# Optimization experiments

Hardware: AMD Instinct MI355X
Metric: run time of the kernel (lower is better)

The kernel has to match this reference:

```python
import jax, jax.numpy as jnp
import numpy as np

N = 512          # max_nodes
H = 256          # hidden_dim
L = 4            # num_layers
T = 100          # num_timesteps
NE = N * (N - 1) // 2  # 130816 upper-triangular edges

# --- cosine noise schedule (computed in float64 numpy, stored as float32) ---
_s = 0.008
_steps = np.arange(T + 1, dtype=np.float64)
_ab = np.cos((_steps / T + _s) / (1 + _s) * np.pi / 2) ** 2
_ab = _ab / _ab[0]
_betas = np.clip(1.0 - _ab[1:] / _ab[:-1], None, 0.999).astype(np.float32)
_alphas = 1.0 - _betas
_alpha_bar = np.cumprod(_alphas).astype(np.float32)
SQRT_AB = jnp.asarray(np.sqrt(_alpha_bar), dtype=jnp.float32)
SQRT_OMAB = jnp.asarray(np.sqrt(1.0 - _alpha_bar), dtype=jnp.float32)
IU, JU = np.triu_indices(N, k=1)  # upper-triangular edge indices


def silu(x):
    return x * jax.nn.sigmoid(x)


def layernorm(x, g, b, eps=1e-5):
    mu = jnp.mean(x, axis=-1, keepdims=True)
    var = jnp.mean(jnp.square(x - mu), axis=-1, keepdims=True)
    return (x - mu) / jnp.sqrt(var + eps) * g + b


def setup_inputs() -> dict:
    key = jax.random.key(0)
    ks = jax.random.split(key, 16)
    B = 32
    p = lambda k, shape: jax.random.normal(k, shape, dtype=jnp.float32) * 0.02
    return {
        "adj_0": jax.random.normal(ks[0], (B, N, N), dtype=jnp.float32),
        "noise": jax.random.normal(ks[1], (B, N, N), dtype=jnp.float32),
        # time embedding MLP: Linear(1,H), SiLU, Linear(H,H)
        "te_W1": p(ks[2], (1, H)), "te_b1": jnp.zeros((H,), jnp.float32),
        "te_W2": p(ks[3], (H, H)), "te_b2": jnp.zeros((H,), jnp.float32),
        # input projection Linear(N, H)
        "ip_W": p(ks[4], (N, H)), "ip_b": jnp.zeros((H,), jnp.float32),
        # per-layer params stacked on leading L axis
        "msg_W": p(ks[5], (L, H, H)), "msg_b": jnp.zeros((L, H), jnp.float32),
        "upd_W": p(ks[6], (L, 2 * H, H)), "upd_b": jnp.zeros((L, H), jnp.float32),
        "ln_g": jnp.ones((L, H), jnp.float32), "ln_b": jnp.zeros((L, H), jnp.float32),
        "tp_W": p(ks[7], (L, H, H)), "tp_b": jnp.zeros((L, H), jnp.float32),
        # output projection: Linear(H,H), SiLU, Linear(H, NE)
        "op_W1": p(ks[8], (H, H)), "op_b1": jnp.zeros((H,), jnp.float32),
        "op_W2": p(ks[9], (H, NE)), "op_b2": jnp.zeros((NE,), jnp.float32),
        "t": jax.random.randint(ks[10], (32,), 0, T),
    }


def reference(adj_0, noise, te_W1, te_b1, te_W2, te_b2, ip_W, ip_b,
              msg_W, msg_b, upd_W, upd_b, ln_g, ln_b, tp_W, tp_b,
              op_W1, op_b1, op_W2, op_b2, t):
    # q_sample: noisy adjacency at timestep t
    adj_t = SQRT_AB[t][:, None, None] * adj_0 + SQRT_OMAB[t][:, None, None] * noise
    # time embedding
    tf = (t.astype(jnp.float32) / T)[:, None]               # [B,1]
    t_emb = silu(tf @ te_W1 + te_b1) @ te_W2 + te_b2        # [B,H]
    # input projection
    h = adj_t @ ip_W + ip_b                                  # [B,N,H]
    # adjacency normalization is identical across layers -> hoist
    adj_norm = adj_t / (jnp.sum(jnp.abs(adj_t), axis=-1, keepdims=True) + 1.0)
    for l in range(L):
        msg = jnp.einsum('bij,bjh->bih', adj_norm, h @ msg_W[l] + msg_b[l])
        t_bias = (t_emb @ tp_W[l] + tp_b[l])[:, None, :]     # [B,1,H]
        h_new = jnp.concatenate([h, msg], axis=-1) @ upd_W[l] + upd_b[l] + t_bias
        h = layernorm(h_new + h, ln_g[l], ln_b[l])
    h_graph = jnp.sum(h, axis=1)                             # [B,H]
    noise_pred = silu(h_graph @ op_W1 + op_b1) @ op_W2 + op_b2  # [B,NE]
    # MSE against the upper-triangular entries of the true noise
    target = noise[:, IU, JU]                                # [B,NE]
    loss = jnp.mean(jnp.square(noise_pred - target))
    return loss
```

## Files before the change

### kernel.cpp

```cpp
#include <hip/hip_runtime.h>
#include <math.h>

#define NN 512
#define HH 256
#define BB 32
#define NE 130816

typedef unsigned short ushort_t;
typedef unsigned int u32;
using short8  = __attribute__((ext_vector_type(8))) short;
using floatx4 = __attribute__((ext_vector_type(4))) float;

typedef __attribute__((address_space(3))) u32* lds_u32p;
typedef const __attribute__((address_space(1))) u32* glb_u32p;

__device__ inline unsigned short f2bf(float f) {
    unsigned int u = __float_as_uint(f);
    unsigned int r = (u + 0x7fffu + ((u >> 16) & 1u)) >> 16;
    return (unsigned short)r;
}
__device__ inline float bf2f(unsigned short x) {
    return __uint_as_float(((unsigned int)x) << 16);
}

__device__ inline float wave_reduce_sum(float v) {
#pragma unroll
    for (int o = 32; o > 0; o >>= 1) v += __shfl_xor(v, o, 64);
    return v;
}
__device__ inline float block_reduce_sum256(float v, float* red) {
    v = wave_reduce_sum(v);
    int w = threadIdx.x >> 6;
    if ((threadIdx.x & 63) == 0) red[w] = v;
    __syncthreads();
    v = red[0] + red[1] + red[2] + red[3];
    __syncthreads();
    return v;
}

__global__ void init_kernel(float* __restrict__ sched, float* __restrict__ out) {
    __shared__ float alpha_s[100];
    int tid = threadIdx.x;
    if (tid < 100) {
        const double PI_H = 3.14159265358979323846 * 0.5;
        double f1 = (((double)tid / 100.0) + 0.008) / 1.008 * PI_H;
        double f2 = (((double)(tid + 1) / 100.0) + 0.008) / 1.008 * PI_H;
        double c1 = cos(f1), c2 = cos(f2);
        double beta = 1.0 - (c2 * c2) / (c1 * c1);
        if (beta > 0.999) beta = 0.999;
        alpha_s[tid] = 1.0f - (float)beta;
    }
    __syncthreads();
    if (tid == 0) {
        out[0] = 0.0f;
        float cum = 1.0f;
        for (int k = 0; k < 100; k++) {
            cum *= alpha_s[k];
            sched[k]       = sqrtf(cum);
            sched[100 + k] = sqrtf(1.0f - cum);
        }
    }
}

__global__ __launch_bounds__(256) void temb1_kernel(
    const float* __restrict__ te_W1, const float* __restrict__ te_b1,
    const float* __restrict__ te_W2, const float* __restrict__ te_b2,
    const int* __restrict__ t, float* __restrict__ emb_out) {
    const int b = blockIdx.x, cb = blockIdx.y * 64, tid = threadIdx.x;
    __shared__ float hid[HH];
    __shared__ float part[4][64];
    float tf = (float)t[b] / 100.0f;
    float z = tf * te_W1[tid] + te_b1[tid];
    hid[tid] = z / (1.0f + expf(-z));
    __syncthreads();
    const int col = tid & 63, kc = tid >> 6;
    float a = 0.0f;
#pragma unroll 8
    for (int k0 = 0; k0 < 64; k0++) {
        int k = kc * 64 + k0;
        a = fmaf(hid[k], te_W2[k * HH + cb + col], a);
    }
    part[kc][col] = a;
    __syncthreads();
    if (kc == 0) {
        float o = part[0][col] + part[1][col] + part[2][col] + part[3][col] + te_b2[cb + col];
        emb_out[b * HH + cb + col] = o;
    }
}

__global__ __launch_bounds__(256) void temb2_kernel(
    const float* __restrict__ emb, const float* __restrict__ tp_W,
    const float* __restrict__ tp_b, float* __restrict__ tbias_out) {
    const int b = blockIdx.x;
    const int l = blockIdx.y >> 2, cb = (blockIdx.y & 3) * 64;
    const int tid = threadIdx.x;
    __shared__ float es[HH];
    __shared__ float part[4][64];
    es[tid] = emb[b * HH + tid];
    __syncthreads();
    const int col = tid & 63, kc = tid >> 6;
    const float* W = tp_W + l * HH * HH;
    float a = 0.0f;
#pragma unroll 8
    for (int k0 = 0; k0 < 64; k0++) {
        int k = kc * 64 + k0;
        a = fmaf(es[k], W[k * HH + cb + col], a);
    }
    part[kc][col] = a;
    __syncthreads();
    if (kc == 0) {
        float o = part[0][col] + part[1][col] + part[2][col] + part[3][col]
                + tp_b[l * HH + cb + col];
        tbias_out[l * (BB * HH) + b * HH + cb + col] = o;
    }
}

__global__ __launch_bounds__(256) void adj_kernel(
    const float* __restrict__ adj0, const float* __restrict__ noise,
    const int* __restrict__ t, const float* __restrict__ sched,
    ushort_t* __restrict__ adjt_bf, float* __restrict__ invrs) {
    __shared__ float red[4];
    const int bid = blockIdx.x;
    const int b = bid >> 9;
    const int ts = t[b];
    const float sab = sched[ts], som = sched[100 + ts];
    const size_t base = (size_t)bid * NN;
    const int tid = threadIdx.x;
    float s = 0.0f;
#pragma unroll
    for (int jj = 0; jj < 2; jj++) {
        int j = tid + jj * 256;
        float a = sab * adj0[base + j] + som * noise[base + j];
        adjt_bf[base + j] = f2bf(a);
        s += fabsf(a);
    }
    s = block_reduce_sum256(s, red);
    if (tid == 0) invrs[bid] = 1.0f / (s + 1.0f);
}

__global__ __launch_bounds__(256) void wcvt_kernel(
    const float* __restrict__ ip_W, const float* __restrict__ msg_W,
    const float* __restrict__ upd_W,
    ushort_t* __restrict__ ipWT, ushort_t* __restrict__ msgWT,
    ushort_t* __restrict__ updWT) {
    const int z = blockIdx.z;
    const float* src; ushort_t* dst; int R;
    if (z == 0)      { src = ip_W;                          dst = ipWT;                       R = 512; }
    else if (z <= 4) { src = msg_W + (z - 1) * 65536;       dst = msgWT + (z - 1) * 65536;    R = 256; }
    else             { src = upd_W + (z - 5) * 131072;      dst = updWT + (z - 5) * 131072;   R = 512; }
    const int r0 = blockIdx.y * 32, c0 = blockIdx.x * 32;
    if (r0 >= R) return;
    __shared__ float T[32][33];
    const int tr = threadIdx.x >> 5, tc = threadIdx.x & 31;
#pragma unroll
    for (int s = 0; s < 32; s += 8)
        T[tr + s][tc] = src[(size_t)(r0 + tr + s) * 256 + c0 + tc];
    __syncthreads();
#pragma unroll
    for (int s = 0; s < 32; s += 8)
        dst[(size_t)(c0 + tr + s) * R + r0 + tc] = f2bf(T[tc][tr + s]);
}

__global__ __launch_bounds__(256, 2) void gemm_bf16(
    int K,
    const ushort_t* __restrict__ A, int lda, const ushort_t* __restrict__ A2,
    const ushort_t* __restrict__ BT, int ldbt, long long bstride,
    const float* __restrict__ bias, const float* __restrict__ scale,
    const float* __restrict__ tbias, const ushort_t* __restrict__ resid,
    float* __restrict__ Cf, ushort_t* __restrict__ Cb, ushort_t* __restrict__ CbT) {
    __shared__ ushort_t As[128 * 32];
    __shared__ ushort_t Bs[64 * 32];
    __shared__ ushort_t Ts[64 * 136];
    const int row0 = blockIdx.x * 128;
    const int n0 = blockIdx.y * 64;
    const int tid = threadIdx.x;
    const int lane = tid & 63;
    const int w = tid >> 6;
    const int l15 = lane & 15, quad = lane >> 4;
    const int wm = (w >> 1) * 64, wn = (w & 1) * 32;
    const ushort_t* Bp = BT + (size_t)(row0 >> 9) * (size_t)bstride;

    const int srow = lane >> 2;
    const int gkoff = (((lane & 3) ^ (lane >> 4)) << 3);
    const int swz = ((quad ^ ((l15 >> 2) & 3)) << 3);

    floatx4 acc[4][2];
#pragma unroll
    for (int i = 0; i < 4; i++)
#pragma unroll
        for (int j = 0; j < 2; j++) {
            acc[i][j][0] = 0.0f; acc[i][j][1] = 0.0f;
            acc[i][j][2] = 0.0f; acc[i][j][3] = 0.0f;
        }

    for (int kc = 0; kc < K; kc += 32) {
        const ushort_t* Ause = A; int kk = kc;
        if (A2 && kc >= 256) { Ause = A2; kk = kc - 256; }
#pragma unroll
        for (int r = 0; r < 2; r++) {
            const int lbase = (r * 4 + w) * 16;
            const ushort_t* gpA = Ause + (size_t)(row0 + lbase + srow) * lda + kk + gkoff;
            __builtin_amdgcn_global_load_lds((glb_u32p)(const void*)gpA,
                                             (lds_u32p)(void*)&As[lbase * 32], 16, 0, 0);
        }
        {
            const int lbase = w * 16;
            const ushort_t* gpB = Bp + (size_t)(n0 + lbase + srow) * ldbt + kc + gkoff;
            __builtin_amdgcn_global_load_lds((glb_u32p)(const void*)gpB,
                                             (lds_u32p)(void*)&Bs[lbase * 32], 16, 0, 0);
        }
        __syncthreads();

        short8 af[4], bfr[2];
#pragma unroll
        for (int tm = 0; tm < 4; tm++)
            af[tm] = *(const short8*)&As[(wm + tm * 16 + l15) * 32 + swz];
#pragma unroll
        for (int tn = 0; tn < 2; tn++)
            bfr[tn] = *(const short8*)&Bs[(wn + tn * 16 + l15) * 32 + swz];
#pragma unroll
        for (int tm = 0; tm < 4; tm++)
#pragma unroll
            for (int tn = 0; tn < 2; tn++)
                acc[tm][tn] = __builtin_amdgcn_mfma_f32_16x16x32_bf16(
                    af[tm], bfr[tn], acc[tm][tn], 0, 0, 0);
        __syncthreads();
    }

    if (CbT) {
#pragma unroll
        for (int tm = 0; tm < 4; tm++)
#pragma unroll
            for (int tn = 0; tn < 2; tn++)
#pragma unroll
                for (int r = 0; r < 4; r++) {
                    const int ml = wm + tm * 16 + quad * 4 + r;
                    const int cl = wn + tn * 16 + l15;
                    float v = acc[tm][tn][r];
                    if (bias) v += bias[n0 + cl];
                    Ts[cl * 136 + ml] = f2bf(v);
                }
        __syncthreads();
        const int cl = tid >> 2, ch = (tid & 3) * 32;
        const int b = row0 >> 9;
        ushort_t* dst = CbT + (size_t)b * NN * HH + (size_t)(n0 + cl) * NN + (row0 & 511) + ch;
        uint4 u0 = *(const uint4*)&Ts[cl * 136 + ch];
        uint4 u1 = *(const uint4*)&Ts[cl * 136 + ch + 8];
        uint4 u2 = *(const uint4*)&Ts[cl * 136 + ch + 16];
        uint4 u3 = *(const uint4*)&Ts[cl * 136 + ch + 24];
        *(uint4*)(dst)      = u0;
        *(uint4*)(dst + 8)  = u1;
        *(uint4*)(dst + 16) = u2;
        *(uint4*)(dst + 24) = u3;
        return;
    }

#pragma unroll
    for (int tm = 0; tm < 4; tm++)
#pragma unroll
        for (int tn = 0; tn < 2; tn++) {
#pragma unroll
            for (int r = 0; r < 4; r++) {
                const int row = row0 + wm + tm * 16 + quad * 4 + r;
                const int col = n0 + wn + tn * 16 + l15;
                float v = acc[tm][tn][r];
                if (scale) v *= scale[row];
                if (bias) v += bias[col];
                if (tbias) v += tbias[((row >> 9) << 8) + col] + bf2f(resid[(size_t)row * HH + col]);
                if (Cf) Cf[(size_t)row * HH + col] = v;
                if (Cb) Cb[(size_t)row * HH + col] = f2bf(v);
            }
        }
}

__global__ __launch_bounds__(256) void ln_kernel(
    const float* __restrict__ pre, const float* __restrict__ g,
    const float* __restrict__ b, ushort_t* __restrict__ h_bf) {
    __shared__ float red[4];
    const size_t base = (size_t)blockIdx.x * HH;
    const int tid = threadIdx.x;
    float x = pre[base + tid];
    float mu = block_reduce_sum256(x, red) * (1.0f / HH);
    float d = x - mu;
    float var = block_reduce_sum256(d * d, red) * (1.0f / HH);
    h_bf[base + tid] = f2bf(d * rsqrtf(var + 1e-5f) * g[tid] + b[tid]);
}

__global__ __launch_bounds__(256) void psum_kernel(
    const ushort_t* __restrict__ h_bf, float* __restrict__ partial) {
    const int b = blockIdx.x, ch = blockIdx.y, tid = threadIdx.x;
    const ushort_t* hp = h_bf + ((size_t)b * NN + ch * 32) * HH;
    float s = 0.0f;
#pragma unroll
    for (int i = 0; i < 32; i++) s += bf2f(hp[i * HH + tid]);
    partial[(((size_t)b * 16 + ch) << 8) + tid] = s;
}

__global__ __launch_bounds__(256) void final_kernel(
    const float* __restrict__ partial, const float* __restrict__ op_W1,
    const float* __restrict__ op_b1, float* __restrict__ sT) {
    int b = blockIdx.x, tid = threadIdx.x;
    __shared__ float hg[HH];
    float acc = 0.0f;
#pragma unroll
    for (int c = 0; c < 16; c++) acc += partial[(((size_t)b * 16 + c) << 8) + tid];
    hg[tid] = acc;
    __syncthreads();
    float o = op_b1[tid];
#pragma unroll 8
    for (int k = 0; k < HH; k++) o = fmaf(hg[k], op_W1[k * HH + tid], o);
    sT[tid * BB + b] = o / (1.0f + expf(-o));
}

__global__ __launch_bounds__(256) void loss_kernel(
    const float* __restrict__ sT, const float* __restrict__ op_W2,
    const float* __restrict__ op_b2, const float* __restrict__ noise,
    float* __restrict__ out) {
    __shared__ float red[4];
    const int tid = threadIdx.x;
    const int e = blockIdx.x * 256 + tid;
    float lsum = 0.0f;
    float acc[32];
#pragma unroll
    for (int b = 0; b < 32; b++) acc[b] = 0.0f;
    const float* w2 = op_W2 + e;
#pragma unroll 8
    for (int h = 0; h < 256; h++) {
        float wv = w2[(size_t)h * NE];
        const float* sr = sT + h * BB;
#pragma unroll
        for (int b = 0; b < 32; b++) acc[b] = fmaf(sr[b], wv, acc[b]);
    }
    int i = (int)((1023.0 - sqrt(1046529.0 - 8.0 * (double)e)) * 0.5);
    if (i < 0) i = 0;
    if (i > 510) i = 510;
    while (i > 0 && (i * (1023 - i)) / 2 > e) --i;
    while (((i + 1) * (1022 - i)) / 2 <= e) ++i;
    int j = i + 1 + (e - (i * (1023 - i)) / 2);
    const float pb = op_b2[e];
    const float* np = noise + (size_t)i * NN + j;
#pragma unroll
    for (int b = 0; b < 32; b++) {
        float d = acc[b] + pb - np[(size_t)b * NN * NN];
        lsum += d * d;
    }
    lsum *= (1.0f / (32.0f * (float)NE));
    lsum = block_reduce_sum256(lsum, red);
    if (tid == 0) atomicAdd(out, lsum);
}

extern "C" void kernel_launch(void* const* d_in, const int* in_sizes, int n_in,
                              void* d_out, int out_size, void* d_ws, size_t ws_size,
                              hipStream_t stream) {
    const float* adj0  = (const float*)d_in[0];
    const float* noise = (const float*)d_in[1];
    const float* te_W1 = (const float*)d_in[2];
    const float* te_b1 = (const float*)d_in[3];
    const float* te_W2 = (const float*)d_in[4];
    const float* te_b2 = (const float*)d_in[5];
    const float* ip_W  = (const float*)d_in[6];
    const float* ip_b  = (const float*)d_in[7];
    const float* msg_W = (const float*)d_in[8];
    const float* msg_b = (const float*)d_in[9];
    const float* upd_W = (const float*)d_in[10];
    const float* upd_b = (const float*)d_in[11];
    const float* ln_g  = (const float*)d_in[12];
    const float* ln_b  = (const float*)d_in[13];
    const float* tp_W  = (const float*)d_in[14];
    const float* tp_b  = (const float*)d_in[15];
    const float* op_W1 = (const float*)d_in[16];
    const float* op_b1 = (const float*)d_in[17];
    const float* op_W2 = (const float*)d_in[18];
    const float* op_b2 = (const float*)d_in[19];
    const int*   t     = (const int*)d_in[20];
    float* out = (float*)d_out;

    float* ws = (float*)d_ws;
    float* sched   = ws;
    float* tbias   = ws + 256;
    float* invrs   = ws + 33024;
    float* sbuf    = ws + 49408;
    float* embb    = ws + 57600;
    float* partial = ws + 65792;
    float* pre     = ws + 196864;
    ushort_t* bfb  = (ushort_t*)(ws + 4391168);
    ushort_t* adjt_bf = bfb;
    ushort_t* h_bf    = bfb + 8388608;
    ushort_t* msg_bf  = bfb + 12582912;
    ushort_t* hmT_bf  = bfb + 16777216;
    ushort_t* ipWT    = bfb + 20971520;
    ushort_t* msgWT   = bfb + 21102592;
    ushort_t* updWT   = bfb + 21364736;

    init_kernel<<<1, 128, 0, stream>>>(sched, out);
    wcvt_kernel<<<dim3(8, 16, 9), 256, 0, stream>>>(ip_W, msg_W, upd_W, ipWT, msgWT, updWT);
    temb1_kernel<<<dim3(32, 4), 256, 0, stream>>>(te_W1, te_b1, te_W2, te_b2, t, embb);
    temb2_kernel<<<dim3(32, 16), 256, 0, stream>>>(embb, tp_W, tp_b, tbias);
    adj_kernel<<<BB * NN, 256, 0, stream>>>(adj0, noise, t, sched, adjt_bf, invrs);

    dim3 ggrid(128, 4);
    gemm_bf16<<<ggrid, 256, 0, stream>>>(512, adjt_bf, 512, nullptr,
                                         ipWT, 512, 0,
                                         ip_b, nullptr, nullptr, nullptr,
                                         nullptr, h_bf, nullptr);
    for (int l = 0; l < 4; l++) {
        gemm_bf16<<<ggrid, 256, 0, stream>>>(256, h_bf, 256, nullptr,
                                             msgWT + l * 65536, 256, 0,
                                             msg_b + l * HH, nullptr, nullptr, nullptr,
                                             nullptr, nullptr, hmT_bf);
        gemm_bf16<<<ggrid, 256, 0, stream>>>(512, adjt_bf, 512, nullptr,
                                             hmT_bf, 512, (long long)(HH * NN),
                                             nullptr, invrs, nullptr, nullptr,
                                             nullptr, msg_bf, nullptr);
        gemm_bf16<<<ggrid, 256, 0, stream>>>(512, h_bf, 256, msg_bf,
                                             updWT + l * 131072, 512, 0,
                                             upd_b + l * HH, nullptr,
                                             tbias + l * BB * HH, h_bf,
                                             pre, nullptr, nullptr);
        ln_kernel<<<BB * NN, 256, 0, stream>>>(pre, ln_g + l * HH, ln_b + l * HH, h_bf);
    }
    psum_kernel<<<dim3(32, 16), 256, 0, stream>>>(h_bf, partial);
    final_kernel<<<32, 256, 0, stream>>>(partial, op_W1, op_b1, sbuf);
    loss_kernel<<<511, 256, 0, stream>>>(sbuf, op_W2, op_b2, noise, out);
}
```

Measured before the change: 632.0 us.

## Fold message weight into update weight to drop one GEMM per layer

The message path concat([h,msg])@upd_W is rewritten algebraically. msg_W is premultiplied into the lower half of upd_W (Wf = msg_W@upd_W[256:]), and the folded msg_b term becomes a bias vector. Each layer then runs one wide GEMM over h that produces both the h-half partial (part1, bf16) and the transposed h@Wf, followed by the adjacency GEMM that fuses scale, bias, partial, time bias and residual. This removes one K=512 GEMM per layer and the msg_bf round trip, at the cost of an extra bf16 rounding of part1 and a changed accumulation order. The adj kernel is also vectorised to float2 loads.

```diff
diff --git a/kernel.cpp b/kernel.cpp
--- a/kernel.cpp
+++ b/kernel.cpp
@@ -126,14 +126,13 @@
     const float sab = sched[ts], som = sched[100 + ts];
     const size_t base = (size_t)bid * NN;
     const int tid = threadIdx.x;
-    float s = 0.0f;
-#pragma unroll
-    for (int jj = 0; jj < 2; jj++) {
-        int j = tid + jj * 256;
-        float a = sab * adj0[base + j] + som * noise[base + j];
-        adjt_bf[base + j] = f2bf(a);
-        s += fabsf(a);
-    }
+    const int j = tid * 2;
+    float2 a0 = *(const float2*)&adj0[base + j];
+    float2 n0 = *(const float2*)&noise[base + j];
+    float x = fmaf(sab, a0.x, som * n0.x);
+    float y = fmaf(sab, a0.y, som * n0.y);
+    *(u32*)&adjt_bf[base + j] = (u32)f2bf(x) | ((u32)f2bf(y) << 16);
+    float s = fabsf(x) + fabsf(y);
     s = block_reduce_sum256(s, red);
     if (tid == 0) invrs[bid] = 1.0f / (s + 1.0f);
 }
@@ -141,17 +140,25 @@
 __global__ __launch_bounds__(256) void wcvt_kernel(
     const float* __restrict__ ip_W, const float* __restrict__ msg_W,
     const float* __restrict__ upd_W,
-    ushort_t* __restrict__ ipWT, ushort_t* __restrict__ msgWT,
+    ushort_t* __restrict__ ipWT, ushort_t* __restrict__ msgWbf,
     ushort_t* __restrict__ updWT) {
     const int z = blockIdx.z;
+    const int r0 = blockIdx.y * 32, c0 = blockIdx.x * 32;
+    const int tr = threadIdx.x >> 5, tc = threadIdx.x & 31;
+    if (z >= 1 && z <= 4) {
+        const float* src = msg_W + (z - 1) * 65536;
+        ushort_t* dst = msgWbf + (z - 1) * 65536;
+        if (r0 >= 256) return;
+#pragma unroll
+        for (int s = 0; s < 32; s += 8)
+            dst[(size_t)(r0 + tr + s) * 256 + c0 + tc] =
+                f2bf(src[(size_t)(r0 + tr + s) * 256 + c0 + tc]);
+        return;
+    }
     const float* src; ushort_t* dst; int R;
-    if (z == 0)      { src = ip_W;                          dst = ipWT;                       R = 512; }
-    else if (z <= 4) { src = msg_W + (z - 1) * 65536;       dst = msgWT + (z - 1) * 65536;    R = 256; }
-    else             { src = upd_W + (z - 5) * 131072;      dst = updWT + (z - 5) * 131072;   R = 512; }
-    const int r0 = blockIdx.y * 32, c0 = blockIdx.x * 32;
-    if (r0 >= R) return;
+    if (z == 0) { src = ip_W;                     dst = ipWT;                     R = 512; }
+    else        { src = upd_W + (z - 5) * 131072; dst = updWT + (z - 5) * 131072; R = 512; }
     __shared__ float T[32][33];
-    const int tr = threadIdx.x >> 5, tc = threadIdx.x & 31;
 #pragma unroll
     for (int s = 0; s < 32; s += 8)
         T[tr + s][tc] = src[(size_t)(r0 + tr + s) * 256 + c0 + tc];
@@ -161,24 +168,47 @@
         dst[(size_t)(c0 + tr + s) * R + r0 + tc] = f2bf(T[tc][tr + s]);
 }
 
+__global__ __launch_bounds__(256) void bfv_kernel(
+    const float* __restrict__ msg_b, const float* __restrict__ upd_W,
+    float* __restrict__ bfv) {
+    const int l = blockIdx.x, n = threadIdx.x;
+    float a = 0.0f;
+#pragma unroll 8
+    for (int j = 0; j < 256; j++)
+        a = fmaf(msg_b[l * 256 + j], upd_W[(size_t)l * 131072 + (size_t)(256 + j) * 256 + n], a);
+    bfv[l * 256 + n] = a;
+}
+
 __global__ __launch_bounds__(256, 2) void gemm_bf16(
-    int K,
-    const ushort_t* __restrict__ A, int lda, const ushort_t* __restrict__ A2,
-    const ushort_t* __restrict__ BT, int ldbt, long long bstride,
-    const float* __restrict__ bias, const float* __restrict__ scale,
+    int K, int nsplit,
+    const ushort_t* __restrict__ A, int lda, long long aStrideZ,
+    const ushort_t* __restrict__ BT, int ldbt,
+    const ushort_t* __restrict__ BT2, int ldbt2,
+    long long btStrideZ, long long bstride,
+    const float* __restrict__ bias, const float* __restrict__ bias2,
+    const float* __restrict__ scale,
     const float* __restrict__ tbias, const ushort_t* __restrict__ resid,
-    float* __restrict__ Cf, ushort_t* __restrict__ Cb, ushort_t* __restrict__ CbT) {
+    const ushort_t* __restrict__ part1,
+    float* __restrict__ Cf, ushort_t* __restrict__ Cb, ushort_t* __restrict__ CbT,
+    long long cStrideZ) {
     __shared__ ushort_t As[128 * 32];
     __shared__ ushort_t Bs[64 * 32];
     __shared__ ushort_t Ts[64 * 136];
     const int row0 = blockIdx.x * 128;
     const int n0 = blockIdx.y * 64;
+    const int z = blockIdx.z;
     const int tid = threadIdx.x;
     const int lane = tid & 63;
     const int w = tid >> 6;
     const int l15 = lane & 15, quad = lane >> 4;
     const int wm = (w >> 1) * 64, wn = (w & 1) * 32;
-    const ushort_t* Bp = BT + (size_t)(row0 >> 9) * (size_t)bstride;
+
+    const bool reg2 = (n0 >= nsplit);
+    const ushort_t* BTu = reg2 ? BT2 : BT;
+    const int ldbtu = reg2 ? ldbt2 : ldbt;
+    const int n0u = reg2 ? (n0 - nsplit) : n0;
+    const ushort_t* Az = A + (size_t)z * aStrideZ;
+    const ushort_t* Bp = BTu + (size_t)z * btStrideZ + (size_t)(row0 >> 9) * (size_t)bstride;
 
     const int srow = lane >> 2;
     const int gkoff = (((lane & 3) ^ (lane >> 4)) << 3);
@@ -194,18 +224,16 @@
         }
 
     for (int kc = 0; kc < K; kc += 32) {
-        const ushort_t* Ause = A; int kk = kc;
-        if (A2 && kc >= 256) { Ause = A2; kk = kc - 256; }
 #pragma unroll
         for (int r = 0; r < 2; r++) {
             const int lbase = (r * 4 + w) * 16;
-            const ushort_t* gpA = Ause + (size_t)(row0 + lbase + srow) * lda + kk + gkoff;
+            const ushort_t* gpA = Az + (size_t)(row0 + lbase + srow) * lda + kc + gkoff;
             __builtin_amdgcn_global_load_lds((glb_u32p)(const void*)gpA,
                                              (lds_u32p)(void*)&As[lbase * 32], 16, 0, 0);
         }
         {
             const int lbase = w * 16;
-            const ushort_t* gpB = Bp + (size_t)(n0 + lbase + srow) * ldbt + kc + gkoff;
+            const ushort_t* gpB = Bp + (size_t)(n0u + lbase + srow) * ldbtu + kc + gkoff;
             __builtin_amdgcn_global_load_lds((glb_u32p)(const void*)gpB,
                                              (lds_u32p)(void*)&Bs[lbase * 32], 16, 0, 0);
         }
@@ -227,7 +255,7 @@
         __syncthreads();
     }
 
-    if (CbT) {
+    if (reg2) {
 #pragma unroll
         for (int tm = 0; tm < 4; tm++)
 #pragma unroll
@@ -237,13 +265,13 @@
                     const int ml = wm + tm * 16 + quad * 4 + r;
                     const int cl = wn + tn * 16 + l15;
                     float v = acc[tm][tn][r];
-                    if (bias) v += bias[n0 + cl];
+                    if (bias2) v += bias2[n0u + cl];
                     Ts[cl * 136 + ml] = f2bf(v);
                 }
         __syncthreads();
         const int cl = tid >> 2, ch = (tid & 3) * 32;
         const int b = row0 >> 9;
-        ushort_t* dst = CbT + (size_t)b * NN * HH + (size_t)(n0 + cl) * NN + (row0 & 511) + ch;
+        ushort_t* dst = CbT + (size_t)b * NN * HH + (size_t)(n0u + cl) * NN + (row0 & 511) + ch;
         uint4 u0 = *(const uint4*)&Ts[cl * 136 + ch];
         uint4 u1 = *(const uint4*)&Ts[cl * 136 + ch + 8];
         uint4 u2 = *(const uint4*)&Ts[cl * 136 + ch + 16];
@@ -266,9 +294,10 @@
                 float v = acc[tm][tn][r];
                 if (scale) v *= scale[row];
                 if (bias) v += bias[col];
+                if (part1) v += bf2f(part1[(size_t)row * HH + col]);
                 if (tbias) v += tbias[((row >> 9) << 8) + col] + bf2f(resid[(size_t)row * HH + col]);
                 if (Cf) Cf[(size_t)row * HH + col] = v;
-                if (Cb) Cb[(size_t)row * HH + col] = f2bf(v);
+                if (Cb) Cb[(size_t)z * cStrideZ + (size_t)row * HH + col] = f2bf(v);
             }
         }
 }
@@ -381,42 +410,57 @@
     float* invrs   = ws + 33024;
     float* sbuf    = ws + 49408;
     float* embb    = ws + 57600;
-    float* partial = ws + 65792;
-    float* pre     = ws + 196864;
-    ushort_t* bfb  = (ushort_t*)(ws + 4391168);
+    float* bfv     = ws + 65792;
+    float* partial = ws + 66816;
+    float* pre     = ws + 197888;
+    ushort_t* bfb  = (ushort_t*)(ws + 4392192);
     ushort_t* adjt_bf = bfb;
     ushort_t* h_bf    = bfb + 8388608;
-    ushort_t* msg_bf  = bfb + 12582912;
-    ushort_t* hmT_bf  = bfb + 16777216;
+    ushort_t* part1   = bfb + 12582912;
+    ushort_t* hm2T    = bfb + 16777216;
     ushort_t* ipWT    = bfb + 20971520;
-    ushort_t* msgWT   = bfb + 21102592;
+    ushort_t* msgWbf  = bfb + 21102592;
     ushort_t* updWT   = bfb + 21364736;
+    ushort_t* WfT     = bfb + 21889024;
+
+    const int NS_OFF = 1 << 30;
 
     init_kernel<<<1, 128, 0, stream>>>(sched, out);
-    wcvt_kernel<<<dim3(8, 16, 9), 256, 0, stream>>>(ip_W, msg_W, upd_W, ipWT, msgWT, updWT);
+    wcvt_kernel<<<dim3(8, 16, 9), 256, 0, stream>>>(ip_W, msg_W, upd_W, ipWT, msgWbf, updWT);
+    bfv_kernel<<<4, 256, 0, stream>>>(msg_b, upd_W, bfv);
     temb1_kernel<<<dim3(32, 4), 256, 0, stream>>>(te_W1, te_b1, te_W2, te_b2, t, embb);
     temb2_kernel<<<dim3(32, 16), 256, 0, stream>>>(embb, tp_W, tp_b, tbias);
     adj_kernel<<<BB * NN, 256, 0, stream>>>(adj0, noise, t, sched, adjt_bf, invrs);
 
-    dim3 ggrid(128, 4);
-    gemm_bf16<<<ggrid, 256, 0, stream>>>(512, adjt_bf, 512, nullptr,
-                                         ipWT, 512, 0,
-                                         ip_b, nullptr, nullptr, nullptr,
-                                         nullptr, h_bf, nullptr);
+    gemm_bf16<<<dim3(2, 4, 4), 256, 0, stream>>>(
+        256, NS_OFF,
+        updWT + 256, 512, 131072,
+        msgWbf, 256, nullptr, 0, 65536, 0,
+        nullptr, nullptr, nullptr, nullptr, nullptr, nullptr,
+        nullptr, WfT, nullptr, 65536);
+
+    gemm_bf16<<<dim3(128, 4), 256, 0, stream>>>(
+        512, NS_OFF,
+        adjt_bf, 512, 0,
+        ipWT, 512, nullptr, 0, 0, 0,
+        ip_b, nullptr, nullptr, nullptr, nullptr, nullptr,
+        nullptr, h_bf, nullptr, 0);
+
     for (int l = 0; l < 4; l++) {
-        gemm_bf16<<<ggrid, 256, 0, stream>>>(256, h_bf, 256, nullptr,
-                                             msgWT + l * 65536, 256, 0,
-                                             msg_b + l * HH, nullptr, nullptr, nullptr,
-                                             nullptr, nullptr, hmT_bf);
-        gemm_bf16<<<ggrid, 256, 0, stream>>>(512, adjt_bf, 512, nullptr,
-                                             hmT_bf, 512, (long long)(HH * NN),
-                                             nullptr, invrs, nullptr, nullptr,
-                                             nullptr, msg_bf, nullptr);
-        gemm_bf16<<<ggrid, 256, 0, stream>>>(512, h_bf, 256, msg_bf,
-                                             updWT + l * 131072, 512, 0,
-                                             upd_b + l * HH, nullptr,
-                                             tbias + l * BB * HH, h_bf,
-                                             pre, nullptr, nullptr);
+        gemm_bf16<<<dim3(128, 8), 256, 0, stream>>>(
+            256, 256,
+            h_bf, 256, 0,
+            updWT + l * 131072, 512,
+            WfT + l * 65536, 256, 0, 0,
+            nullptr, bfv + l * 256, nullptr, nullptr, nullptr, nullptr,
+            nullptr, part1, hm2T, 0);
+        gemm_bf16<<<dim3(128, 4), 256, 0, stream>>>(
+            512, NS_OFF,
+            adjt_bf, 512, 0,
+            hm2T, 512, nullptr, 0, 0, (long long)(HH * NN),
+            upd_b + l * HH, nullptr, invrs,
+            tbias + l * BB * HH, h_bf, part1,
+            pre, nullptr, nullptr, 0);
         ln_kernel<<<BB * NN, 256, 0, stream>>>(pre, ln_g + l * HH, ln_b + l * HH, h_bf);
     }
     psum_kernel<<<dim3(32, 16), 256, 0, stream>>>(h_bf, partial);
```

After: 636.3 us. About the same (+0.7%).
